# Performance work log

Measured on AMD Instinct MI355X. Metric: run time of the kernel, lower is better.

## Reference

```python
import jax, jax.numpy as jnp
import numpy as np

WS, SS, P, H = 7, 3, 14, 12  # window, shift, patch grid, heads
NW = (P // WS) ** 2          # windows per image = 4
N_WIN = WS * WS              # tokens per window = 49

def _rel_pos_index():
    coords = np.stack(np.meshgrid(np.arange(WS), np.arange(WS), indexing='ij')).reshape(2, -1)
    rel = (coords[:, :, None] - coords[:, None, :]).transpose(1, 2, 0).astype(np.int64)
    rel[..., 0] += WS - 1
    rel[..., 1] += WS - 1
    rel[..., 0] *= 2 * WS - 1
    return rel.sum(-1)  # [49,49]

def _shift_mask():
    img = np.zeros((P, P))
    sl = (slice(0, -WS), slice(-WS, -SS), slice(-SS, None))
    cnt = 0
    for h in sl:
        for w in sl:
            img[h, w] = cnt
            cnt += 1
    mw = img.reshape(P // WS, WS, P // WS, WS).transpose(0, 2, 1, 3).reshape(-1, N_WIN)
    am = mw[:, None, :] - mw[:, :, None]
    return np.where(am != 0, -100.0, 0.0).astype(np.float32)  # [nW,49,49]

RPI = jnp.asarray(_rel_pos_index())
MASK = jnp.asarray(_shift_mask())

def _hswish(x):
    return x * jnp.clip(x + 3.0, 0.0, 6.0) / 6.0

def _hsig(x):
    return jnp.clip(x + 3.0, 0.0, 6.0) / 6.0

def _bn(x, g, b, eps=1e-5):
    # training-mode batchnorm over (B,H,W) per channel, biased variance
    m = x.mean((0, 2, 3), keepdims=True)
    v = ((x - m) ** 2).mean((0, 2, 3), keepdims=True)
    return (x - m) / jnp.sqrt(v + eps) * g[None, :, None, None] + b[None, :, None, None]

def setup_inputs() -> dict:
    key = jax.random.key(0)
    ks = jax.random.split(key, 20)
    C, HID = 768, 3072
    return {
        'x': jax.random.normal(ks[0], (32, 197, C), jnp.float32),
        'w_qkv': jax.random.normal(ks[1], (3 * C, C), jnp.float32) * 0.02,
        'w_proj': jax.random.normal(ks[2], (C, C), jnp.float32) * 0.02,
        'b_proj': jax.random.normal(ks[3], (C,), jnp.float32) * 0.02,
        'rpb_table': jax.random.normal(ks[4], ((2 * WS - 1) ** 2, H), jnp.float32) * 0.02,
        'pw1_w': jax.random.normal(ks[5], (HID, C), jnp.float32) * 0.02,
        'bn1_g': 1.0 + jax.random.normal(ks[6], (HID,), jnp.float32) * 0.02,
        'bn1_b': jax.random.normal(ks[7], (HID,), jnp.float32) * 0.02,
        'dw_w': jax.random.normal(ks[8], (HID, 3, 3), jnp.float32) * 0.1,
        'bn2_g': 1.0 + jax.random.normal(ks[9], (HID,), jnp.float32) * 0.02,
        'bn2_b': jax.random.normal(ks[10], (HID,), jnp.float32) * 0.02,
        'se_w1': jax.random.normal(ks[11], (HID // 4, HID), jnp.float32) * 0.02,
        'se_b1': jax.random.normal(ks[12], (HID // 4,), jnp.float32) * 0.02,
        'se_w2': jax.random.normal(ks[13], (HID, HID // 4), jnp.float32) * 0.02,
        'se_b2': jax.random.normal(ks[14], (HID,), jnp.float32) * 0.02,
        'pw2_w': jax.random.normal(ks[15], (C, HID), jnp.float32) * 0.02,
        'bn3_g': 1.0 + jax.random.normal(ks[16], (C,), jnp.float32) * 0.02,
        'bn3_b': jax.random.normal(ks[17], (C,), jnp.float32) * 0.02,
    }

def reference(x, w_qkv, w_proj, b_proj, rpb_table, pw1_w, bn1_g, bn1_b, dw_w,
              bn2_g, bn2_b, se_w1, se_b1, se_w2, se_b2, pw2_w, bn3_g, bn3_b):
    B, N, C = x.shape
    hd = C // H
    scale = hd ** -0.5
    nw = P // WS

    cls_tok = x[:, :1]
    xs = x[:, 1:].reshape(B, P, P, C)
    xs = jnp.roll(xs, (-SS, -SS), axis=(1, 2))  # cyclic shift
    # window partition -> [B*nW, 49, C]
    win = xs.reshape(B, nw, WS, nw, WS, C).transpose(0, 1, 3, 2, 4, 5).reshape(B * NW, N_WIN, C)

    qkv = (win @ w_qkv.T).reshape(B * NW, N_WIN, 3, H, hd).transpose(2, 0, 3, 1, 4)
    q, k, v = qkv[0], qkv[1], qkv[2]  # [B*nW, H, 49, hd]
    attn = jnp.einsum('bhqd,bhkd->bhqk', q, k) * scale
    # relative position bias gather: [H,49,49]
    bias = rpb_table[RPI.reshape(-1)].reshape(N_WIN, N_WIN, H).transpose(2, 0, 1)
    attn = attn + bias[None]
    # shifted-window mask add
    attn = (attn.reshape(B, NW, H, N_WIN, N_WIN) + MASK[None, :, None]).reshape(B * NW, H, N_WIN, N_WIN)
    attn = jax.nn.softmax(attn, axis=-1)
    out = jnp.einsum('bhqk,bhkd->bhqd', attn, v).transpose(0, 2, 1, 3).reshape(B * NW, N_WIN, C)
    out = out @ w_proj.T + b_proj

    # window reverse + reverse shift
    xs = out.reshape(B, nw, nw, WS, WS, C).transpose(0, 1, 3, 2, 4, 5).reshape(B, P, P, C)
    xs = jnp.roll(xs, (SS, SS), axis=(1, 2))
    x = jnp.concatenate([cls_tok, xs.reshape(B, P * P, C)], axis=1)

    # LocalityFeedForward (inverted residual conv MLP with SE)
    cls_tok, xt = x[:, :1], x[:, 1:]
    f = xt.transpose(0, 2, 1).reshape(B, C, P, P)
    h = _hswish(_bn(jnp.einsum('bchw,oc->bohw', f, pw1_w), bn1_g, bn1_b))
    h = _hswish(_bn(jax.lax.conv_general_dilated(
        h, dw_w[:, None], (1, 1), 'SAME',
        feature_group_count=h.shape[1],
        dimension_numbers=('NCHW', 'OIHW', 'NCHW')), bn2_g, bn2_b))
    s = h.mean((2, 3))  # global avg pool [B, hid]
    s = _hsig(jax.nn.relu(s @ se_w1.T + se_b1) @ se_w2.T + se_b2)
    h = h * s[:, :, None, None]
    h = _bn(jnp.einsum('bchw,oc->bohw', h, pw2_w), bn3_g, bn3_b)
    f = f + h
    x = jnp.concatenate([cls_tok, f.reshape(B, C, P * P).transpose(0, 2, 1)], axis=1)
    return x
```

## Files before the change

kernel.cpp:

```cpp
#include <hip/hip_runtime.h>
#include <hip/hip_bf16.h>

typedef unsigned short ushort_t;
typedef unsigned int uint_t;
typedef short short8 __attribute__((ext_vector_type(8)));
typedef float floatx4 __attribute__((ext_vector_type(4)));

__device__ inline float b2f(ushort_t u){
    uint_t v = ((uint_t)u) << 16;
    return __uint_as_float(v);
}
__device__ inline ushort_t f2b(float f){
    uint_t v = __float_as_uint(f);
    uint_t r = (v + 0x7FFFu + ((v >> 16) & 1u)) >> 16;
    return (ushort_t)r;
}
__device__ inline void unpack8(uint4 u, float* f){
    uint_t w[4] = {u.x, u.y, u.z, u.w};
    #pragma unroll
    for (int i = 0; i < 4; ++i){
        f[2*i]   = __uint_as_float(w[i] << 16);
        f[2*i+1] = __uint_as_float(w[i] & 0xFFFF0000u);
    }
}
__device__ inline uint4 pack8(const float* f){
    uint4 o;
    uint_t w[4];
    #pragma unroll
    for (int i = 0; i < 4; ++i)
        w[i] = (uint_t)f2b(f[2*i]) | ((uint_t)f2b(f[2*i+1]) << 16);
    o.x = w[0]; o.y = w[1]; o.z = w[2]; o.w = w[3];
    return o;
}
__device__ inline ushort4 cvt4(float4 v){
    ushort4 o;
    o.x = f2b(v.x); o.y = f2b(v.y); o.z = f2b(v.z); o.w = f2b(v.w);
    return o;
}
__device__ inline float hswish(float y){
    return y * fminf(fmaxf(y + 3.f, 0.f), 6.f) * (1.f/6.f);
}

#define MROWS 6272
#define CDIM  768
#define HID   3072
#define QKV3  2304

__device__ inline int scatter_row(int ri){
    int w  = ri / 49, t = ri % 49;
    int b  = w >> 2,  wi = w & 3;
    int wy = wi >> 1, wx = wi & 1;
    int ty = t / 7,   tx = t % 7;
    int yd = (wy*7 + ty + 3) % 14;
    int xd = (wx*7 + tx + 3) % 14;
    return b*196 + yd*14 + xd;
}

__global__ __launch_bounds__(256) void cvt_f2b(const float4* __restrict__ in,
                                               ushort4* __restrict__ out, int n4){
    int i = blockIdx.x * 256 + threadIdx.x;
    if (i < n4) out[i] = cvt4(in[i]);
}

__global__ __launch_bounds__(256) void dw_transpose(const float* __restrict__ w,
                                                    float* __restrict__ wT){
    int i = blockIdx.x*256 + threadIdx.x;
    if (i < HID*9){ int c = i/9, k = i%9; wT[k*HID + c] = w[i]; }
}

__global__ __launch_bounds__(256) void gather_win(const float4* __restrict__ x,
                                                  ushort4* __restrict__ win){
    int idx = blockIdx.x * 256 + threadIdx.x;
    if (idx >= MROWS * 192) return;
    int r  = idx / 192, c4 = idx % 192;
    int w  = r / 49,  t  = r % 49;
    int b  = w >> 2,  wi = w & 3;
    int wy = wi >> 1, wx = wi & 1;
    int ty = t / 7,   tx = t % 7;
    int ys = (wy*7 + ty + 3) % 14;
    int xs = (wx*7 + tx + 3) % 14;
    win[idx] = cvt4(x[(size_t)b*197*192 + (size_t)(1 + ys*14 + xs)*192 + c4]);
}

__global__ __launch_bounds__(256) void gemm_bt(const ushort_t* __restrict__ A,
                                               const ushort_t* __restrict__ B,
                                               ushort_t* __restrict__ Cb,
                                               float* __restrict__ Cf,
                                               int M, int N, int K,
                                               const float* __restrict__ bias,
                                               float* __restrict__ stats,
                                               int scat){
    const int nx   = gridDim.x;
    int flat = blockIdx.y * nx + blockIdx.x;
    int xcd  = flat & 7;
    int k    = flat >> 3;
    int by   = xcd + 8 * (k / nx);
    int bx   = k % nx;
    if (by * 128 >= M) return;

    __shared__ __align__(16) ushort_t As[2][128*32];
    __shared__ __align__(16) ushort_t Bs[2][128*32];
    const int tid  = threadIdx.x;
    const int lane = tid & 63;
    const int wid  = tid >> 6;
    const int m0 = by * 128;
    const int n0 = bx * 128;
    const int wm = (wid >> 1) * 64;
    const int wn = (wid & 1) * 64;

    const int srow = (lane >> 2);
    const int scol = (((lane & 3) ^ ((lane >> 3) & 3)) * 8);

    floatx4 acc[4][4] = {};

    auto stage = [&](int buf, int k0){
        #pragma unroll
        for (int j = 0; j < 2; ++j){
            int ch  = wid*2 + j;
            const ushort_t* gA = A + (size_t)(m0 + ch*16 + srow)*K + k0 + scol;
            const ushort_t* gB = B + (size_t)(n0 + ch*16 + srow)*K + k0 + scol;
            __builtin_amdgcn_global_load_lds(
                (const __attribute__((address_space(1))) void*)gA,
                (__attribute__((address_space(3))) void*)(&As[buf][ch*512 + lane*8]), 16, 0, 0);
            __builtin_amdgcn_global_load_lds(
                (const __attribute__((address_space(1))) void*)gB,
                (__attribute__((address_space(3))) void*)(&Bs[buf][ch*512 + lane*8]), 16, 0, 0);
        }
    };

    const int NK = K >> 5;
    stage(0, 0);

    const int fr   = lane & 15;
    const int quad = lane >> 4;
    const int cosw = (quad ^ ((fr >> 1) & 3)) * 8;
    int cur = 0;
    for (int it = 0; it < NK; ++it){
        __builtin_amdgcn_sched_barrier(0);
        __builtin_amdgcn_s_barrier();
        if (it + 1 < NK){
            stage(cur ^ 1, (it + 1) << 5);
            asm volatile("s_waitcnt vmcnt(4)" ::: "memory");
        } else {
            asm volatile("s_waitcnt vmcnt(0)" ::: "memory");
        }
        __builtin_amdgcn_s_barrier();
        __builtin_amdgcn_sched_barrier(0);

        short8 af[4], bfr[4];
        #pragma unroll
        for (int i = 0; i < 4; ++i){
            af[i]  = *(const short8*)(&As[cur][(wm + i*16 + fr)*32 + cosw]);
            bfr[i] = *(const short8*)(&Bs[cur][(wn + i*16 + fr)*32 + cosw]);
        }
        #pragma unroll
        for (int i = 0; i < 4; ++i)
            #pragma unroll
            for (int j = 0; j < 4; ++j)
                acc[i][j] = __builtin_amdgcn_mfma_f32_16x16x32_bf16(af[i], bfr[j], acc[i][j], 0, 0, 0);
        cur ^= 1;
    }

    if (!scat && Cb){
        __syncthreads();
        ushort_t* Cspace = (wid < 2) ? &As[0][0] : &Bs[0][0];
        #pragma unroll
        for (int i = 0; i < 4; ++i){
            #pragma unroll
            for (int j = 0; j < 4; ++j){
                int col = wn + j*16 + fr;
                float bv = bias ? bias[n0 + col] : 0.f;
                #pragma unroll
                for (int r = 0; r < 4; ++r)
                    Cspace[(i*16 + quad*4 + r)*128 + (col ^ (quad << 4))] =
                        f2b(acc[i][j][r] + bv);
            }
        }
        __syncthreads();
        #pragma unroll
        for (int q = 0; q < 8; ++q){
            int fl  = q*256 + tid;
            int row = fl >> 4, u4c = fl & 15;
            const ushort_t* srcRow = (row < 64) ? (&As[0][0] + row*128)
                                                : (&Bs[0][0] + (row - 64)*128);
            int g = (row >> 2) & 3;
            *(uint4*)(Cb + (size_t)(m0 + row)*N + n0 + u4c*8) =
                *(const uint4*)(srcRow + ((u4c*8) ^ (g << 4)));
        }
    } else {
        #pragma unroll
        for (int i = 0; i < 4; ++i){
            int grow = m0 + wm + i*16 + quad*4;
            #pragma unroll
            for (int j = 0; j < 4; ++j){
                int gcol = n0 + wn + j*16 + fr;
                float bv = bias ? bias[gcol] : 0.f;
                if (scat){
                    #pragma unroll
                    for (int r = 0; r < 4; ++r){
                        float v = acc[i][j][r] + bv;
                        size_t off = (size_t)scatter_row(grow + r)*N + gcol;
                        if (Cf) Cf[off] = v;
                        Cb[off] = f2b(v);
                    }
                } else {
                    #pragma unroll
                    for (int r = 0; r < 4; ++r)
                        Cf[(size_t)(grow + r)*N + gcol] = acc[i][j][r] + bv;
                }
            }
        }
    }

    if (stats){
        #pragma unroll
        for (int j = 0; j < 4; ++j){
            int gcol = n0 + wn + j*16 + fr;
            float bv = bias ? bias[gcol] : 0.f;
            float sv = 0.f, sq = 0.f;
            #pragma unroll
            for (int i = 0; i < 4; ++i)
                #pragma unroll
                for (int r = 0; r < 4; ++r){
                    float v = acc[i][j][r] + bv;
                    sv += v; sq += v*v;
                }
            sv += __shfl_xor(sv, 16, 64);  sq += __shfl_xor(sq, 16, 64);
            sv += __shfl_xor(sv, 32, 64);  sq += __shfl_xor(sq, 32, 64);
            if (lane < 16){
                atomicAdd(&stats[gcol], sv);
                atomicAdd(&stats[N + gcol], sq);
            }
        }
    }
}

__global__ __launch_bounds__(256) void gemm_bt64(const ushort_t* __restrict__ A,
                                                 const ushort_t* __restrict__ B,
                                                 ushort_t* __restrict__ Cb,
                                                 float* __restrict__ Cf,
                                                 int M, int N, int K,
                                                 const float* __restrict__ bias,
                                                 float* __restrict__ stats,
                                                 int scat){
    const int nx   = gridDim.x;
    int flat = blockIdx.y * nx + blockIdx.x;
    int xcd  = flat & 7;
    int k    = flat >> 3;
    int by   = xcd + 8 * (k / nx);
    int bx   = k % nx;
    if (by * 128 >= M) return;

    __shared__ __align__(16) ushort_t As[2][128*32];
    __shared__ __align__(16) ushort_t Bs[2][64*32];
    const int tid  = threadIdx.x;
    const int lane = tid & 63;
    const int wid  = tid >> 6;
    const int m0 = by * 128;
    const int n0 = bx * 64;
    const int wm = (wid >> 1) * 64;
    const int wn = (wid & 1) * 32;

    const int srow = (lane >> 2);
    const int scol = (((lane & 3) ^ ((lane >> 3) & 3)) * 8);

    floatx4 acc[4][2] = {};

    auto stage = [&](int buf, int k0){
        #pragma unroll
        for (int j = 0; j < 2; ++j){
            int ch = wid*2 + j;
            const ushort_t* gA = A + (size_t)(m0 + ch*16 + srow)*K + k0 + scol;
            __builtin_amdgcn_global_load_lds(
                (const __attribute__((address_space(1))) void*)gA,
                (__attribute__((address_space(3))) void*)(&As[buf][ch*512 + lane*8]), 16, 0, 0);
        }
        const ushort_t* gB = B + (size_t)(n0 + wid*16 + srow)*K + k0 + scol;
        __builtin_amdgcn_global_load_lds(
            (const __attribute__((address_space(1))) void*)gB,
            (__attribute__((address_space(3))) void*)(&Bs[buf][wid*512 + lane*8]), 16, 0, 0);
    };

    const int NK = K >> 5;
    stage(0, 0);

    const int fr   = lane & 15;
    const int quad = lane >> 4;
    const int cosw = (quad ^ ((fr >> 1) & 3)) * 8;
    int cur = 0;
    for (int it = 0; it < NK; ++it){
        __builtin_amdgcn_sched_barrier(0);
        __builtin_amdgcn_s_barrier();
        if (it + 1 < NK){
            stage(cur ^ 1, (it + 1) << 5);
            asm volatile("s_waitcnt vmcnt(3)" ::: "memory");
        } else {
            asm volatile("s_waitcnt vmcnt(0)" ::: "memory");
        }
        __builtin_amdgcn_s_barrier();
        __builtin_amdgcn_sched_barrier(0);

        short8 af[4], bfr[2];
        #pragma unroll
        for (int i = 0; i < 4; ++i)
            af[i]  = *(const short8*)(&As[cur][(wm + i*16 + fr)*32 + cosw]);
        #pragma unroll
        for (int j = 0; j < 2; ++j)
            bfr[j] = *(const short8*)(&Bs[cur][(wn + j*16 + fr)*32 + cosw]);
        #pragma unroll
        for (int i = 0; i < 4; ++i)
            #pragma unroll
            for (int j = 0; j < 2; ++j)
                acc[i][j] = __builtin_amdgcn_mfma_f32_16x16x32_bf16(af[i], bfr[j], acc[i][j], 0, 0, 0);
        cur ^= 1;
    }

    if (!scat && Cb){
        __syncthreads();
        ushort_t* Cst = &As[0][0];
        #pragma unroll
        for (int i = 0; i < 4; ++i){
            #pragma unroll
            for (int j = 0; j < 2; ++j){
                int col = wn + j*16 + fr;
                float bv = bias ? bias[n0 + col] : 0.f;
                #pragma unroll
                for (int r = 0; r < 4; ++r)
                    Cst[(wm + i*16 + quad*4 + r)*64 + (col ^ (quad << 4))] =
                        f2b(acc[i][j][r] + bv);
            }
        }
        __syncthreads();
        #pragma unroll
        for (int q = 0; q < 4; ++q){
            int fl  = q*256 + tid;
            int row = fl >> 3, u4c = fl & 7;
            int g = (row >> 2) & 3;
            *(uint4*)(Cb + (size_t)(m0 + row)*N + n0 + u4c*8) =
                *(const uint4*)(Cst + row*64 + ((u4c*8) ^ (g << 4)));
        }
    } else {
        #pragma unroll
        for (int i = 0; i < 4; ++i){
            int grow = m0 + wm + i*16 + quad*4;
            #pragma unroll
            for (int j = 0; j < 2; ++j){
                int gcol = n0 + wn + j*16 + fr;
                float bv = bias ? bias[gcol] : 0.f;
                if (scat){
                    #pragma unroll
                    for (int r = 0; r < 4; ++r){
                        float v = acc[i][j][r] + bv;
                        size_t off = (size_t)scatter_row(grow + r)*N + gcol;
                        if (Cf) Cf[off] = v;
                        Cb[off] = f2b(v);
                    }
                } else {
                    #pragma unroll
                    for (int r = 0; r < 4; ++r)
                        Cf[(size_t)(grow + r)*N + gcol] = acc[i][j][r] + bv;
                }
            }
        }
    }

    if (stats){
        #pragma unroll
        for (int j = 0; j < 2; ++j){
            int gcol = n0 + wn + j*16 + fr;
            float bv = bias ? bias[gcol] : 0.f;
            float sv = 0.f, sq = 0.f;
            #pragma unroll
            for (int i = 0; i < 4; ++i)
                #pragma unroll
                for (int r = 0; r < 4; ++r){
                    float v = acc[i][j][r] + bv;
                    sv += v; sq += v*v;
                }
            sv += __shfl_xor(sv, 16, 64);  sq += __shfl_xor(sq, 16, 64);
            sv += __shfl_xor(sv, 32, 64);  sq += __shfl_xor(sq, 32, 64);
            if (lane < 16){
                atomicAdd(&stats[gcol], sv);
                atomicAdd(&stats[N + gcol], sq);
            }
        }
    }
}

__global__ __launch_bounds__(256) void bm_precompute(const float* __restrict__ rpb,
                                                     float* __restrict__ bm){
    int idx = blockIdx.x*256 + threadIdx.x;
    if (idx >= 12*4*64*64) return;
    int ki = idx & 63, qi = (idx >> 6) & 63, wi = (idx >> 12) & 3, h = idx >> 14;
    float v = -1e30f;
    if (qi < 49 && ki < 49){
        int qy = qi/7, qx = qi%7, ky = ki/7, kx = ki%7;
        int ridx = (qy - ky + 6)*13 + (qx - kx + 6);
        v = rpb[ridx*12 + h];
        int wy = wi >> 1, wx = wi & 1;
        int gqy = wy*7 + qy, gqx = wx*7 + qx, gky = wy*7 + ky, gkx = wx*7 + kx;
        int cq = ((gqy < 7) ? 0 : (gqy < 11 ? 1 : 2))*3 + ((gqx < 7) ? 0 : (gqx < 11 ? 1 : 2));
        int ck = ((gky < 7) ? 0 : (gky < 11 ? 1 : 2))*3 + ((gkx < 7) ? 0 : (gkx < 11 ? 1 : 2));
        if (cq != ck) v -= 100.f;
    }
    bm[idx] = v;
}

__global__ __launch_bounds__(256) void attn_mfma(const ushort_t* __restrict__ qkv,
                                                 ushort_t* __restrict__ outp,
                                                 const float* __restrict__ bm){
    __shared__ __align__(16) ushort_t Ps[64*72];
    __shared__ __align__(16) ushort_t VT[64*72];
    const int tid = threadIdx.x, lane = tid & 63, wid = tid >> 6;
    const int h = blockIdx.x, w = blockIdx.y, wi = w & 3;
    const int fr = lane & 15, quad = lane >> 4, co = quad*8;

    for (int idx = tid; idx < 64*8; idx += 256){
        int k = idx >> 3, ng = idx & 7;
        uint4 u = {0u, 0u, 0u, 0u};
        if (k < 49) u = *(const uint4*)(qkv + (size_t)(w*49 + k)*QKV3 + 1536 + h*64 + ng*8);
        const ushort_t* vp = (const ushort_t*)&u;
        #pragma unroll
        for (int e = 0; e < 8; ++e) VT[(ng*8 + e)*72 + k] = vp[e];
    }
    __syncthreads();

    floatx4 accs[4] = {};
    const ushort_t* qbase = qkv + (size_t)(w*49 + wid*16 + fr)*QKV3 + h*64;
    #pragma unroll
    for (int k0 = 0; k0 < 64; k0 += 32){
        short8 af = *(const short8*)(qbase + k0 + co);
        #pragma unroll
        for (int j = 0; j < 4; ++j){
            const ushort_t* kbase = qkv + (size_t)(w*49 + j*16 + fr)*QKV3 + 768 + h*64;
            short8 bf = *(const short8*)(kbase + k0 + co);
            accs[j] = __builtin_amdgcn_mfma_f32_16x16x32_bf16(af, bf, accs[j], 0, 0, 0);
        }
    }

    const float* bmh = bm + (size_t)((h*4 + wi)*64 + wid*16)*64;
    #pragma unroll
    for (int r = 0; r < 4; ++r){
        int lrow = quad*4 + r;
        float m = -3e38f;
        #pragma unroll
        for (int j = 0; j < 4; ++j){
            float a = accs[j][r]*0.125f + bmh[lrow*64 + j*16 + fr];
            accs[j][r] = a;
            m = fmaxf(m, a);
        }
        #pragma unroll
        for (int off = 1; off < 16; off <<= 1) m = fmaxf(m, __shfl_xor(m, off, 64));
        float s = 0.f;
        #pragma unroll
        for (int j = 0; j < 4; ++j){
            float e = __expf(accs[j][r] - m);
            accs[j][r] = e; s += e;
        }
        #pragma unroll
        for (int off = 1; off < 16; off <<= 1) s += __shfl_xor(s, off, 64);
        float inv = 1.f / s;
        #pragma unroll
        for (int j = 0; j < 4; ++j)
            Ps[(wid*16 + lrow)*72 + j*16 + fr] = f2b(accs[j][r]*inv);
    }
    __syncthreads();

    floatx4 acco[4] = {};
    #pragma unroll
    for (int k0 = 0; k0 < 64; k0 += 32){
        short8 af = *(const short8*)(Ps + (wid*16 + fr)*72 + k0 + co);
        #pragma unroll
        for (int j = 0; j < 4; ++j){
            short8 bf = *(const short8*)(VT + (j*16 + fr)*72 + k0 + co);
            acco[j] = __builtin_amdgcn_mfma_f32_16x16x32_bf16(af, bf, acco[j], 0, 0, 0);
        }
    }
    #pragma unroll
    for (int r = 0; r < 4; ++r){
        int qi = wid*16 + quad*4 + r;
        if (qi < 49){
            #pragma unroll
            for (int j = 0; j < 4; ++j)
                outp[(size_t)(w*49 + qi)*CDIM + h*64 + j*16 + fr] = f2b(acco[j][r]);
        }
    }
}

__global__ void zero_f32(float* __restrict__ p, int n){
    int i = blockIdx.x*256 + threadIdx.x;
    if (i < n) p[i] = 0.f;
}
__global__ void bn_finalize(float* __restrict__ sums, const float* __restrict__ g,
                            const float* __restrict__ b, int Cch){
    int c = blockIdx.x*256 + threadIdx.x;
    if (c >= Cch) return;
    float mean = sums[c] * (1.f/6272.f);
    float var  = sums[Cch + c] * (1.f/6272.f) - mean*mean;
    float sc = g[c] * rsqrtf(var + 1e-5f);
    sums[c] = sc;
    sums[Cch + c] = b[c] - mean*sc;
}

__global__ __launch_bounds__(256) void dwconv_s(const ushort_t* __restrict__ in,
                                                const float* __restrict__ wT,
                                                const float* __restrict__ ss,
                                                ushort_t* __restrict__ out,
                                                float* __restrict__ sums){
    const int cgl = threadIdx.x & 31;
    const int rp  = threadIdx.x >> 5;
    const int cg  = blockIdx.x*32 + cgl;
    const int c   = cg*8;
    const int r0  = blockIdx.y*112;
    float sc[8], sh[8];
    #pragma unroll
    for (int e = 0; e < 8; ++e){ sc[e] = ss[c+e]; sh[e] = ss[HID+c+e]; }
    float wv[9][8];
    #pragma unroll
    for (int kk = 0; kk < 9; ++kk){
        const float4* wp = (const float4*)(wT + kk*HID + c);
        float4 w0 = wp[0], w1 = wp[1];
        wv[kk][0]=w0.x; wv[kk][1]=w0.y; wv[kk][2]=w0.z; wv[kk][3]=w0.w;
        wv[kk][4]=w1.x; wv[kk][5]=w1.y; wv[kk][6]=w1.z; wv[kk][7]=w1.w;
    }
    float s[8] = {}, q[8] = {};
    for (int r = r0 + rp; r < r0 + 112; r += 8){
        int b = r / 196, p = r % 196;
        int y = p / 14,  x = p % 14;
        const uint4* inb = (const uint4*)(in + (size_t)b*196*HID);
        float acc[8] = {};
        #pragma unroll
        for (int ky = 0; ky < 3; ++ky){
            int yy = y + ky - 1;
            if ((unsigned)yy >= 14u) continue;
            #pragma unroll
            for (int kx = 0; kx < 3; ++kx){
                int xx = x + kx - 1;
                if ((unsigned)xx >= 14u) continue;
                uint4 u = inb[(yy*14 + xx)*384 + cg];
                float fin[8]; unpack8(u, fin);
                #pragma unroll
                for (int e = 0; e < 8; ++e)
                    acc[e] += hswish(fin[e]*sc[e] + sh[e]) * wv[ky*3 + kx][e];
            }
        }
        ((uint4*)out)[(size_t)r*384 + cg] = pack8(acc);
        #pragma unroll
        for (int e = 0; e < 8; ++e){ s[e] += acc[e]; q[e] += acc[e]*acc[e]; }
    }
    #pragma unroll
    for (int e = 0; e < 8; ++e){
        s[e] += __shfl_xor(s[e], 32, 64);
        q[e] += __shfl_xor(q[e], 32, 64);
    }
    __shared__ float red[4][32][17];
    const int wvv = threadIdx.x >> 6;
    if ((threadIdx.x & 32) == 0){
        #pragma unroll
        for (int e = 0; e < 8; ++e){
            red[wvv][cgl][e]   = s[e];
            red[wvv][cgl][8+e] = q[e];
        }
    }
    __syncthreads();
    #pragma unroll
    for (int k = 0; k < 2; ++k){
        int o = threadIdx.x*2 + k;
        int cgo = o >> 4, e = o & 15;
        float v = red[0][cgo][e] + red[1][cgo][e] + red[2][cgo][e] + red[3][cgo][e];
        int cc = blockIdx.x*256 + cgo*8 + (e & 7);
        atomicAdd(&sums[(e < 8 ? 0 : HID) + cc], v);
    }
}

__global__ __launch_bounds__(256) void se_mean_v(const ushort_t* __restrict__ X,
                                                 const float* __restrict__ ss,
                                                 float* __restrict__ s){
    const int b   = blockIdx.x;
    const int cgl = threadIdx.x & 31;
    const int rp  = threadIdx.x >> 5;
    const int cg  = blockIdx.y*32 + cgl;
    const int c   = cg*8;
    float sc[8], sh[8];
    #pragma unroll
    for (int e = 0; e < 8; ++e){ sc[e] = ss[c+e]; sh[e] = ss[HID+c+e]; }
    const uint4* Xb = (const uint4*)(X + (size_t)b*196*HID);
    float a[8] = {};
    for (int p = rp; p < 196; p += 8){
        uint4 u = Xb[(size_t)p*384 + cg];
        float f[8]; unpack8(u, f);
        #pragma unroll
        for (int e = 0; e < 8; ++e) a[e] += hswish(f[e]*sc[e] + sh[e]);
    }
    #pragma unroll
    for (int e = 0; e < 8; ++e) a[e] += __shfl_xor(a[e], 32, 64);
    __shared__ float red[4][32][9];
    const int wv = threadIdx.x >> 6;
    if ((threadIdx.x & 32) == 0){
        #pragma unroll
        for (int e = 0; e < 8; ++e) red[wv][cgl][e] = a[e];
    }
    __syncthreads();
    {
        int o = threadIdx.x;
        int cgo = o >> 3, e = o & 7;
        float v = red[0][cgo][e] + red[1][cgo][e] + red[2][cgo][e] + red[3][cgo][e];
        s[(size_t)b*HID + blockIdx.y*256 + cgo*8 + e] = v * (1.f/196.f);
    }
}
__global__ __launch_bounds__(256) void se_fc(const float* __restrict__ in,
                                             const float* __restrict__ w,
                                             const float* __restrict__ bias,
                                             float* __restrict__ out,
                                             int IN, int OUT, int mode){
    int wv   = (blockIdx.x*256 + threadIdx.x) >> 6;
    int lane = threadIdx.x & 63;
    if (wv >= OUT) return;
    const float* wr = w + (size_t)wv * IN;
    float acc[32];
    #pragma unroll
    for (int b = 0; b < 32; ++b) acc[b] = 0.f;
    for (int k = lane; k < IN; k += 64){
        float wval = wr[k];
        #pragma unroll
        for (int b = 0; b < 32; ++b)
            acc[b] += in[b*IN + k] * wval;
    }
    #pragma unroll
    for (int b = 0; b < 32; ++b){
        float v = acc[b];
        #pragma unroll
        for (int off = 32; off; off >>= 1) v += __shfl_down(v, off, 64);
        if (lane == 0){
            float a = v + bias[wv];
            if (mode == 0) a = fmaxf(a, 0.f);
            else           a = fminf(fmaxf(a + 3.f, 0.f), 6.f) * (1.f/6.f);
            out[b*OUT + wv] = a;
        }
    }
}
__global__ __launch_bounds__(256) void se_scale(ushort_t* __restrict__ X,
                                                const float* __restrict__ ss,
                                                const float* __restrict__ s2){
    int idx = blockIdx.x*256 + threadIdx.x;
    if (idx >= MROWS * (HID/8)) return;
    int r = idx / (HID/8), c8 = idx % (HID/8);
    int b = r / 196;
    int c = c8*8;
    uint4 u = ((uint4*)X)[idx];
    float f[8]; unpack8(u, f);
    const float* sp = s2 + b*HID + c;
    #pragma unroll
    for (int e = 0; e < 8; ++e)
        f[e] = hswish(f[e]*ss[c+e] + ss[HID+c+e]) * sp[e];
    ((uint4*)X)[idx] = pack8(f);
}

__global__ __launch_bounds__(256) void final_k(const float4* __restrict__ xin,
                                               const ushort_t* __restrict__ fb,
                                               const ushort_t* __restrict__ hb4,
                                               const float* __restrict__ ss,
                                               float4* __restrict__ outp){
    int idx = blockIdx.x*256 + threadIdx.x;
    if (idx >= 32*197*96) return;
    int b = idx / (197*96);
    int rem = idx % (197*96);
    int n = rem / 96, c8 = rem % 96;
    size_t obase = ((size_t)b*197 + n)*192 + c8*2;
    if (n == 0){
        outp[obase]     = xin[obase];
        outp[obase + 1] = xin[obase + 1];
        return;
    }
    size_t off = ((size_t)b*196 + n - 1)*96 + c8;
    uint4 fu = ((const uint4*)fb)[off];
    uint4 hu = ((const uint4*)hb4)[off];
    float fv[8], hv[8];
    unpack8(fu, fv); unpack8(hu, hv);
    int c = c8*8;
    float4 o0, o1;
    o0.x = fv[0] + hv[0]*ss[c+0] + ss[CDIM + c+0];
    o0.y = fv[1] + hv[1]*ss[c+1] + ss[CDIM + c+1];
    o0.z = fv[2] + hv[2]*ss[c+2] + ss[CDIM + c+2];
    o0.w = fv[3] + hv[3]*ss[c+3] + ss[CDIM + c+3];
    o1.x = fv[4] + hv[4]*ss[c+4] + ss[CDIM + c+4];
    o1.y = fv[5] + hv[5]*ss[c+5] + ss[CDIM + c+5];
    o1.z = fv[6] + hv[6]*ss[c+6] + ss[CDIM + c+6];
    o1.w = fv[7] + hv[7]*ss[c+7] + ss[CDIM + c+7];
    outp[obase]     = o0;
    outp[obase + 1] = o1;
}

extern "C" void kernel_launch(void* const* d_in, const int* in_sizes, int n_in,
                              void* d_out, int out_size, void* d_ws, size_t ws_size,
                              hipStream_t stream){
    const float* x      = (const float*)d_in[0];
    const float* w_qkv  = (const float*)d_in[1];
    const float* w_proj = (const float*)d_in[2];
    const float* b_proj = (const float*)d_in[3];
    const float* rpb    = (const float*)d_in[4];
    const float* pw1_w  = (const float*)d_in[5];
    const float* bn1_g  = (const float*)d_in[6];
    const float* bn1_b  = (const float*)d_in[7];
    const float* dw_w   = (const float*)d_in[8];
    const float* bn2_g  = (const float*)d_in[9];
    const float* bn2_b  = (const float*)d_in[10];
    const float* se_w1  = (const float*)d_in[11];
    const float* se_b1  = (const float*)d_in[12];
    const float* se_w2  = (const float*)d_in[13];
    const float* se_b2  = (const float*)d_in[14];
    const float* pw2_w  = (const float*)d_in[15];
    const float* bn3_g  = (const float*)d_in[16];
    const float* bn3_b  = (const float*)d_in[17];

    char* ws = (char*)d_ws;
    ushort_t* win    = (ushort_t*)(ws + 0);
    float*    bm     = (float*)(ws + 0);
    ushort_t* hb     = (ushort_t*)(ws + 0);
    ushort_t* qkv    = (ushort_t*)(ws + 9633792);
    ushort_t* pw1b   = (ushort_t*)(ws + 9633792);
    ushort_t* wqkvb  = (ushort_t*)(ws + 38535168);
    ushort_t* attnb  = (ushort_t*)(ws + 38535168);
    ushort_t* ha     = (ushort_t*)(ws + 38535168);
    ushort_t* hb4    = (ushort_t*)(ws + 38535168);
    ushort_t* wprojb = (ushort_t*)(ws + 48168960);
    ushort_t* pw2b   = (ushort_t*)(ws + 57802752);
    ushort_t* fb2    = (ushort_t*)(ws + 77070336);
    float*    stats2 = (float*)(ws + 86704128);
    float*    stats3 = (float*)(ws + 86728704);
    float*    stats  = (float*)(ws + 96337920);
    float*    s      = (float*)(ws + 96362496);
    float*    s1     = (float*)(ws + 96755712);
    float*    s2     = (float*)(ws + 96854016);
    float*    dwwT   = (float*)(ws + 96854016);

    const int vec_rows = (MROWS*192 + 255)/256;
    const int vec_hid8 = (MROWS*(HID/8) + 255)/256;
    const int GY = 56;

    zero_f32<<<24, 256, 0, stream>>>(stats, 2*HID);
    zero_f32<<<27, 256, 0, stream>>>(stats2, 2*HID + 2*CDIM);
    dw_transpose<<<(HID*9 + 255)/256, 256, 0, stream>>>(dw_w, dwwT);
    cvt_f2b<<<(QKV3*CDIM/4 + 255)/256, 256, 0, stream>>>((const float4*)w_qkv, (ushort4*)wqkvb, QKV3*CDIM/4);
    cvt_f2b<<<(CDIM*CDIM/4 + 255)/256, 256, 0, stream>>>((const float4*)w_proj, (ushort4*)wprojb, CDIM*CDIM/4);

    gather_win<<<vec_rows, 256, 0, stream>>>((const float4*)x, (ushort4*)win);
    gemm_bt<<<dim3(QKV3/128, GY), 256, 0, stream>>>(win, wqkvb, qkv, nullptr, MROWS, QKV3, CDIM, nullptr, nullptr, 0);
    bm_precompute<<<(12*4*64*64)/256, 256, 0, stream>>>(rpb, bm);
    attn_mfma<<<dim3(12, 128), 256, 0, stream>>>(qkv, attnb, bm);
    cvt_f2b<<<(HID*CDIM/4 + 255)/256, 256, 0, stream>>>((const float4*)pw1_w, (ushort4*)pw1b, HID*CDIM/4);
    gemm_bt64<<<dim3(CDIM/64, GY), 256, 0, stream>>>(attnb, wprojb, fb2, nullptr, MROWS, CDIM, CDIM, b_proj, nullptr, 1);

    gemm_bt<<<dim3(HID/128, GY), 256, 0, stream>>>(fb2, pw1b, ha, nullptr, MROWS, HID, CDIM, nullptr, stats, 0);
    bn_finalize<<<HID/256, 256, 0, stream>>>(stats, bn1_g, bn1_b, HID);

    dwconv_s<<<dim3(12, GY), 256, 0, stream>>>(ha, dwwT, stats, hb, stats2);
    cvt_f2b<<<(CDIM*HID/4 + 255)/256, 256, 0, stream>>>((const float4*)pw2_w, (ushort4*)pw2b, CDIM*HID/4);
    bn_finalize<<<HID/256, 256, 0, stream>>>(stats2, bn2_g, bn2_b, HID);

    se_mean_v<<<dim3(32, 12), 256, 0, stream>>>(hb, stats2, s);
    se_fc<<<dim3((CDIM*64)/256), 256, 0, stream>>>(s, se_w1, se_b1, s1, HID, CDIM, 0);
    se_fc<<<dim3((HID*64)/256), 256, 0, stream>>>(s1, se_w2, se_b2, s2, CDIM, HID, 1);
    se_scale<<<vec_hid8, 256, 0, stream>>>(hb, stats2, s2);

    gemm_bt64<<<dim3(CDIM/64, GY), 256, 0, stream>>>(hb, pw2b, hb4, nullptr, MROWS, CDIM, HID, nullptr, stats3, 0);
    bn_finalize<<<CDIM/256, 256, 0, stream>>>(stats3, bn3_g, bn3_b, CDIM);
    final_k<<<(32*197*96 + 255)/256, 256, 0, stream>>>((const float4*)x, fb2, hb4, stats3, (float4*)d_out);
}
```

Baseline: 521.8 us.

## Split-K the final pointwise GEMM and fold BN finalize into consumers

The last 768-wide, K=3072 GEMM is split into two K halves. Each half atomically accumulates into a zeroed fp32 buffer, and a new combine kernel converts that buffer to bf16 and gathers the BN3 statistics. The separate bn_finalize launches are removed; each consumer kernel now computes scale and shift inline from the raw sums. Weight conversions are moved up front, and the workspace is relaid so buffers do not alias. The goal is to double the block count for the under-filled GEMM and cut launches, at the price of fp32 atomics, an extra zero pass over a ~19MB buffer, and redundant per-thread BN coefficient math.

```diff
diff --git a/kernel.cpp b/kernel.cpp
--- a/kernel.cpp
+++ b/kernel.cpp
@@ -54,6 +54,16 @@
     int yd = (wy*7 + ty + 3) % 14;
     int xd = (wx*7 + tx + 3) % 14;
     return b*196 + yd*14 + xd;
+}
+
+__device__ inline void bn_coef(const float* __restrict__ sums, int Cch,
+                               const float* __restrict__ g, const float* __restrict__ b,
+                               int c, float& sc, float& sh){
+    float mean = sums[c] * (1.f/6272.f);
+    float var  = sums[Cch + c] * (1.f/6272.f) - mean*mean;
+    float s = g[c] * rsqrtf(var + 1e-5f);
+    sc = s;
+    sh = b[c] - mean*s;
 }
 
 __global__ __launch_bounds__(256) void cvt_f2b(const float4* __restrict__ in,
@@ -387,6 +397,137 @@
     }
 }
 
+__global__ __launch_bounds__(256) void gemm_bt64_sk(const ushort_t* __restrict__ A,
+                                                    const ushort_t* __restrict__ B,
+                                                    float* __restrict__ P,
+                                                    int M, int N, int K){
+    const int nx   = gridDim.x;
+    int flat = blockIdx.y * nx + blockIdx.x;
+    int xcd  = flat & 7;
+    int k    = flat >> 3;
+    int by   = xcd + 8 * (k / nx);
+    int bx   = k % nx;
+    if (by * 128 >= M) return;
+    const int kbeg = blockIdx.z * (K >> 1);
+
+    __shared__ __align__(16) ushort_t As[2][128*32];
+    __shared__ __align__(16) ushort_t Bs[2][64*32];
+    const int tid  = threadIdx.x;
+    const int lane = tid & 63;
+    const int wid  = tid >> 6;
+    const int m0 = by * 128;
+    const int n0 = bx * 64;
+    const int wm = (wid >> 1) * 64;
+    const int wn = (wid & 1) * 32;
+
+    const int srow = (lane >> 2);
+    const int scol = (((lane & 3) ^ ((lane >> 3) & 3)) * 8);
+
+    floatx4 acc[4][2] = {};
+
+    auto stage = [&](int buf, int k0){
+        #pragma unroll
+        for (int j = 0; j < 2; ++j){
+            int ch = wid*2 + j;
+            const ushort_t* gA = A + (size_t)(m0 + ch*16 + srow)*K + kbeg + k0 + scol;
+            __builtin_amdgcn_global_load_lds(
+                (const __attribute__((address_space(1))) void*)gA,
+                (__attribute__((address_space(3))) void*)(&As[buf][ch*512 + lane*8]), 16, 0, 0);
+        }
+        const ushort_t* gB = B + (size_t)(n0 + wid*16 + srow)*K + kbeg + k0 + scol;
+        __builtin_amdgcn_global_load_lds(
+            (const __attribute__((address_space(1))) void*)gB,
+            (__attribute__((address_space(3))) void*)(&Bs[buf][wid*512 + lane*8]), 16, 0, 0);
+    };
+
+    const int NK = K >> 6;
+    stage(0, 0);
+
+    const int fr   = lane & 15;
+    const int quad = lane >> 4;
+    const int cosw = (quad ^ ((fr >> 1) & 3)) * 8;
+    int cur = 0;
+    for (int it = 0; it < NK; ++it){
+        __builtin_amdgcn_sched_barrier(0);
+        __builtin_amdgcn_s_barrier();
+        if (it + 1 < NK){
+            stage(cur ^ 1, (it + 1) << 5);
+            asm volatile("s_waitcnt vmcnt(3)" ::: "memory");
+        } else {
+            asm volatile("s_waitcnt vmcnt(0)" ::: "memory");
+        }
+        __builtin_amdgcn_s_barrier();
+        __builtin_amdgcn_sched_barrier(0);
+
+        short8 af[4], bfr[2];
+        #pragma unroll
+        for (int i = 0; i < 4; ++i)
+            af[i]  = *(const short8*)(&As[cur][(wm + i*16 + fr)*32 + cosw]);
+        #pragma unroll
+        for (int j = 0; j < 2; ++j)
+            bfr[j] = *(const short8*)(&Bs[cur][(wn + j*16 + fr)*32 + cosw]);
+        #pragma unroll
+        for (int i = 0; i < 4; ++i)
+            #pragma unroll
+            for (int j = 0; j < 2; ++j)
+                acc[i][j] = __builtin_amdgcn_mfma_f32_16x16x32_bf16(af[i], bfr[j], acc[i][j], 0, 0, 0);
+        cur ^= 1;
+    }
+
+    #pragma unroll
+    for (int i = 0; i < 4; ++i){
+        int grow = m0 + wm + i*16 + quad*4;
+        #pragma unroll
+        for (int j = 0; j < 2; ++j){
+            int gcol = n0 + wn + j*16 + fr;
+            #pragma unroll
+            for (int r = 0; r < 4; ++r)
+                atomicAdd(&P[(size_t)(grow + r)*N + gcol], acc[i][j][r]);
+        }
+    }
+}
+
+__global__ __launch_bounds__(256) void combine_k(const float* __restrict__ p,
+                                                 ushort_t* __restrict__ outb,
+                                                 float* __restrict__ sums){
+    const int cgl = threadIdx.x & 31;
+    const int rp  = threadIdx.x >> 5;
+    const int cg  = blockIdx.x*32 + cgl;
+    const int r0  = blockIdx.y*224;
+    float s[8] = {}, q[8] = {};
+    for (int r = r0 + rp; r < r0 + 224; r += 8){
+        const float4* pr = (const float4*)(p + (size_t)r*CDIM + cg*8);
+        float4 a = pr[0], b = pr[1];
+        float f[8] = {a.x,a.y,a.z,a.w,b.x,b.y,b.z,b.w};
+        #pragma unroll
+        for (int e = 0; e < 8; ++e){ s[e] += f[e]; q[e] += f[e]*f[e]; }
+        ((uint4*)outb)[(size_t)r*96 + cg] = pack8(f);
+    }
+    #pragma unroll
+    for (int e = 0; e < 8; ++e){
+        s[e] += __shfl_xor(s[e], 32, 64);
+        q[e] += __shfl_xor(q[e], 32, 64);
+    }
+    __shared__ float red[4][32][17];
+    const int wv = threadIdx.x >> 6;
+    if ((threadIdx.x & 32) == 0){
+        #pragma unroll
+        for (int e = 0; e < 8; ++e){
+            red[wv][cgl][e]   = s[e];
+            red[wv][cgl][8+e] = q[e];
+        }
+    }
+    __syncthreads();
+    #pragma unroll
+    for (int k = 0; k < 2; ++k){
+        int o = threadIdx.x*2 + k;
+        int cgo = o >> 4, e = o & 15;
+        float v = red[0][cgo][e] + red[1][cgo][e] + red[2][cgo][e] + red[3][cgo][e];
+        int c = blockIdx.x*256 + cgo*8 + (e & 7);
+        atomicAdd(&sums[(e < 8 ? 0 : CDIM) + c], v);
+    }
+}
+
 __global__ __launch_bounds__(256) void bm_precompute(const float* __restrict__ rpb,
                                                      float* __restrict__ bm){
     int idx = blockIdx.x*256 + threadIdx.x;
@@ -491,22 +632,14 @@
     int i = blockIdx.x*256 + threadIdx.x;
     if (i < n) p[i] = 0.f;
 }
-__global__ void bn_finalize(float* __restrict__ sums, const float* __restrict__ g,
-                            const float* __restrict__ b, int Cch){
-    int c = blockIdx.x*256 + threadIdx.x;
-    if (c >= Cch) return;
-    float mean = sums[c] * (1.f/6272.f);
-    float var  = sums[Cch + c] * (1.f/6272.f) - mean*mean;
-    float sc = g[c] * rsqrtf(var + 1e-5f);
-    sums[c] = sc;
-    sums[Cch + c] = b[c] - mean*sc;
-}
 
 __global__ __launch_bounds__(256) void dwconv_s(const ushort_t* __restrict__ in,
                                                 const float* __restrict__ wT,
-                                                const float* __restrict__ ss,
+                                                const float* __restrict__ sums1,
+                                                const float* __restrict__ g1,
+                                                const float* __restrict__ b1,
                                                 ushort_t* __restrict__ out,
-                                                float* __restrict__ sums){
+                                                float* __restrict__ sums2){
     const int cgl = threadIdx.x & 31;
     const int rp  = threadIdx.x >> 5;
     const int cg  = blockIdx.x*32 + cgl;
@@ -514,7 +647,7 @@
     const int r0  = blockIdx.y*112;
     float sc[8], sh[8];
     #pragma unroll
-    for (int e = 0; e < 8; ++e){ sc[e] = ss[c+e]; sh[e] = ss[HID+c+e]; }
+    for (int e = 0; e < 8; ++e) bn_coef(sums1, HID, g1, b1, c+e, sc[e], sh[e]);
     float wv[9][8];
     #pragma unroll
     for (int kk = 0; kk < 9; ++kk){
@@ -569,12 +702,14 @@
         int cgo = o >> 4, e = o & 15;
         float v = red[0][cgo][e] + red[1][cgo][e] + red[2][cgo][e] + red[3][cgo][e];
         int cc = blockIdx.x*256 + cgo*8 + (e & 7);
-        atomicAdd(&sums[(e < 8 ? 0 : HID) + cc], v);
+        atomicAdd(&sums2[(e < 8 ? 0 : HID) + cc], v);
     }
 }
 
 __global__ __launch_bounds__(256) void se_mean_v(const ushort_t* __restrict__ X,
-                                                 const float* __restrict__ ss,
+                                                 const float* __restrict__ sums2,
+                                                 const float* __restrict__ g2,
+                                                 const float* __restrict__ b2,
                                                  float* __restrict__ s){
     const int b   = blockIdx.x;
     const int cgl = threadIdx.x & 31;
@@ -583,7 +718,7 @@
     const int c   = cg*8;
     float sc[8], sh[8];
     #pragma unroll
-    for (int e = 0; e < 8; ++e){ sc[e] = ss[c+e]; sh[e] = ss[HID+c+e]; }
+    for (int e = 0; e < 8; ++e) bn_coef(sums2, HID, g2, b2, c+e, sc[e], sh[e]);
     const uint4* Xb = (const uint4*)(X + (size_t)b*196*HID);
     float a[8] = {};
     for (int p = rp; p < 196; p += 8){
@@ -640,7 +775,9 @@
     }
 }
 __global__ __launch_bounds__(256) void se_scale(ushort_t* __restrict__ X,
-                                                const float* __restrict__ ss,
+                                                const float* __restrict__ sums2,
+                                                const float* __restrict__ g2,
+                                                const float* __restrict__ b2,
                                                 const float* __restrict__ s2){
     int idx = blockIdx.x*256 + threadIdx.x;
     if (idx >= MROWS * (HID/8)) return;
@@ -651,15 +788,20 @@
     float f[8]; unpack8(u, f);
     const float* sp = s2 + b*HID + c;
     #pragma unroll
-    for (int e = 0; e < 8; ++e)
-        f[e] = hswish(f[e]*ss[c+e] + ss[HID+c+e]) * sp[e];
+    for (int e = 0; e < 8; ++e){
+        float sc, sh;
+        bn_coef(sums2, HID, g2, b2, c+e, sc, sh);
+        f[e] = hswish(f[e]*sc + sh) * sp[e];
+    }
     ((uint4*)X)[idx] = pack8(f);
 }
 
 __global__ __launch_bounds__(256) void final_k(const float4* __restrict__ xin,
                                                const ushort_t* __restrict__ fb,
                                                const ushort_t* __restrict__ hb4,
-                                               const float* __restrict__ ss,
+                                               const float* __restrict__ sums3,
+                                               const float* __restrict__ g3,
+                                               const float* __restrict__ b3,
                                                float4* __restrict__ outp){
     int idx = blockIdx.x*256 + threadIdx.x;
     if (idx >= 32*197*96) return;
@@ -678,15 +820,15 @@
     float fv[8], hv[8];
     unpack8(fu, fv); unpack8(hu, hv);
     int c = c8*8;
-    float4 o0, o1;
-    o0.x = fv[0] + hv[0]*ss[c+0] + ss[CDIM + c+0];
-    o0.y = fv[1] + hv[1]*ss[c+1] + ss[CDIM + c+1];
-    o0.z = fv[2] + hv[2]*ss[c+2] + ss[CDIM + c+2];
-    o0.w = fv[3] + hv[3]*ss[c+3] + ss[CDIM + c+3];
-    o1.x = fv[4] + hv[4]*ss[c+4] + ss[CDIM + c+4];
-    o1.y = fv[5] + hv[5]*ss[c+5] + ss[CDIM + c+5];
-    o1.z = fv[6] + hv[6]*ss[c+6] + ss[CDIM + c+6];
-    o1.w = fv[7] + hv[7]*ss[c+7] + ss[CDIM + c+7];
+    float o[8];
+    #pragma unroll
+    for (int e = 0; e < 8; ++e){
+        float sc, sh;
+        bn_coef(sums3, CDIM, g3, b3, c+e, sc, sh);
+        o[e] = fv[e] + hv[e]*sc + sh;
+    }
+    float4 o0 = {o[0], o[1], o[2], o[3]};
+    float4 o1 = {o[4], o[5], o[6], o[7]};
     outp[obase]     = o0;
     outp[obase + 1] = o1;
 }
@@ -715,55 +857,52 @@
 
     char* ws = (char*)d_ws;
     ushort_t* win    = (ushort_t*)(ws + 0);
+    ushort_t* pw1b   = (ushort_t*)(ws + 9633792);
+    ushort_t* wprojb = (ushort_t*)(ws + 14352384);
+    ushort_t* wqkvb  = (ushort_t*)(ws + 15532032);
     float*    bm     = (float*)(ws + 0);
     ushort_t* hb     = (ushort_t*)(ws + 0);
-    ushort_t* qkv    = (ushort_t*)(ws + 9633792);
-    ushort_t* pw1b   = (ushort_t*)(ws + 9633792);
-    ushort_t* wqkvb  = (ushort_t*)(ws + 38535168);
-    ushort_t* attnb  = (ushort_t*)(ws + 38535168);
+    ushort_t* qkv    = (ushort_t*)(ws + 38535168);
+    ushort_t* attnb  = (ushort_t*)(ws + 67436544);
     ushort_t* ha     = (ushort_t*)(ws + 38535168);
-    ushort_t* hb4    = (ushort_t*)(ws + 38535168);
-    ushort_t* wprojb = (ushort_t*)(ws + 48168960);
-    ushort_t* pw2b   = (ushort_t*)(ws + 57802752);
+    float*    p      = (float*)(ws + 38535168);
+    ushort_t* hb4    = (ushort_t*)(ws + 57802752);
     ushort_t* fb2    = (ushort_t*)(ws + 77070336);
-    float*    stats2 = (float*)(ws + 86704128);
-    float*    stats3 = (float*)(ws + 86728704);
-    float*    stats  = (float*)(ws + 96337920);
-    float*    s      = (float*)(ws + 96362496);
-    float*    s1     = (float*)(ws + 96755712);
-    float*    s2     = (float*)(ws + 96854016);
-    float*    dwwT   = (float*)(ws + 96854016);
+    ushort_t* pw2b   = (ushort_t*)(ws + 86704128);
+    float*    dwwT   = (float*)(ws + 91422720);
+    float*    sums2  = (float*)(ws + 91533312);
+    float*    sums3  = (float*)(ws + 91557888);
+    float*    sums1  = (float*)(ws + 91564032);
+    float*    s      = (float*)(ws + 91588608);
+    float*    s1     = (float*)(ws + 91981824);
+    float*    s2     = (float*)(ws + 92080128);
 
     const int vec_rows = (MROWS*192 + 255)/256;
     const int vec_hid8 = (MROWS*(HID/8) + 255)/256;
     const int GY = 56;
 
-    zero_f32<<<24, 256, 0, stream>>>(stats, 2*HID);
-    zero_f32<<<27, 256, 0, stream>>>(stats2, 2*HID + 2*CDIM);
+    zero_f32<<<(2*HID + 2*CDIM + 2*HID + 255)/256, 256, 0, stream>>>(sums2, 2*HID + 2*CDIM + 2*HID);
     dw_transpose<<<(HID*9 + 255)/256, 256, 0, stream>>>(dw_w, dwwT);
     cvt_f2b<<<(QKV3*CDIM/4 + 255)/256, 256, 0, stream>>>((const float4*)w_qkv, (ushort4*)wqkvb, QKV3*CDIM/4);
     cvt_f2b<<<(CDIM*CDIM/4 + 255)/256, 256, 0, stream>>>((const float4*)w_proj, (ushort4*)wprojb, CDIM*CDIM/4);
+    cvt_f2b<<<(HID*CDIM/4 + 255)/256, 256, 0, stream>>>((const float4*)pw1_w, (ushort4*)pw1b, HID*CDIM/4);
+    cvt_f2b<<<(CDIM*HID/4 + 255)/256, 256, 0, stream>>>((const float4*)pw2_w, (ushort4*)pw2b, CDIM*HID/4);
 
     gather_win<<<vec_rows, 256, 0, stream>>>((const float4*)x, (ushort4*)win);
     gemm_bt<<<dim3(QKV3/128, GY), 256, 0, stream>>>(win, wqkvb, qkv, nullptr, MROWS, QKV3, CDIM, nullptr, nullptr, 0);
     bm_precompute<<<(12*4*64*64)/256, 256, 0, stream>>>(rpb, bm);
     attn_mfma<<<dim3(12, 128), 256, 0, stream>>>(qkv, attnb, bm);
-    cvt_f2b<<<(HID*CDIM/4 + 255)/256, 256, 0, stream>>>((const float4*)pw1_w, (ushort4*)pw1b, HID*CDIM/4);
     gemm_bt64<<<dim3(CDIM/64, GY), 256, 0, stream>>>(attnb, wprojb, fb2, nullptr, MROWS, CDIM, CDIM, b_proj, nullptr, 1);
 
-    gemm_bt<<<dim3(HID/128, GY), 256, 0, stream>>>(fb2, pw1b, ha, nullptr, MROWS, HID, CDIM, nullptr, stats, 0);
-    bn_finalize<<<HID/256, 256, 0, stream>>>(stats, bn1_g, bn1_b, HID);
-
-    dwconv_s<<<dim3(12, GY), 256, 0, stream>>>(ha, dwwT, stats, hb, stats2);
-    cvt_f2b<<<(CDIM*HID/4 + 255)/256, 256, 0, stream>>>((const float4*)pw2_w, (ushort4*)pw2b, CDIM*HID/4);
-    bn_finalize<<<HID/256, 256, 0, stream>>>(stats2, bn2_g, bn2_b, HID);
-
-    se_mean_v<<<dim3(32, 12), 256, 0, stream>>>(hb, stats2, s);
+    gemm_bt<<<dim3(HID/128, GY), 256, 0, stream>>>(fb2, pw1b, ha, nullptr, MROWS, HID, CDIM, nullptr, sums1, 0);
+    dwconv_s<<<dim3(12, GY), 256, 0, stream>>>(ha, dwwT, sums1, bn1_g, bn1_b, hb, sums2);
+    zero_f32<<<(MROWS*CDIM + 255)/256, 256, 0, stream>>>(p, MROWS*CDIM);
+    se_mean_v<<<dim3(32, 12), 256, 0, stream>>>(hb, sums2, bn2_g, bn2_b, s);
     se_fc<<<dim3((CDIM*64)/256), 256, 0, stream>>>(s, se_w1, se_b1, s1, HID, CDIM, 0);
     se_fc<<<dim3((HID*64)/256), 256, 0, stream>>>(s1, se_w2, se_b2, s2, CDIM, HID, 1);
-    se_scale<<<vec_hid8, 256, 0, stream>>>(hb, stats2, s2);
-
-    gemm_bt64<<<dim3(CDIM/64, GY), 256, 0, stream>>>(hb, pw2b, hb4, nullptr, MROWS, CDIM, HID, nullptr, stats3, 0);
-    bn_finalize<<<CDIM/256, 256, 0, stream>>>(stats3, bn3_g, bn3_b, CDIM);
-    final_k<<<(32*197*96 + 255)/256, 256, 0, stream>>>((const float4*)x, fb2, hb4, stats3, (float4*)d_out);
-}
+    se_scale<<<vec_hid8, 256, 0, stream>>>(hb, sums2, bn2_g, bn2_b, s2);
+
+    gemm_bt64_sk<<<dim3(CDIM/64, GY, 2), 256, 0, stream>>>(hb, pw2b, p, MROWS, CDIM, HID);
+    combine_k<<<dim3(3, 28), 256, 0, stream>>>(p, hb4, sums3);
+    final_k<<<(32*197*96 + 255)/256, 256, 0, stream>>>((const float4*)x, fb2, hb4, sums3, bn3_g, bn3_b, (float4*)d_out);
+}
```

Result: slower. 563.1 us (+7.9%).
